# Performance work log

Measured on AMD Instinct MI355X. Metric: run time of the kernel, lower is better.

Reference implementation:

```python
import jax, jax.numpy as jnp
from jax import lax
import numpy as np

C = 64
K = 3  # kernel_size
PAD = K // 2


def setup_inputs() -> dict:
    key = jax.random.key(0)
    k1, k2, k3, k4, k5 = jax.random.split(key, 5)
    B, N, H, W = 2, 16, 96, 96
    x = jax.random.normal(k1, (B, C, N, H, W), dtype=jnp.float32)
    # offset conv: Conv2d(C, 2K, kernel=(1,K)) -> 1D conv weight (2K, C, K)
    w_off = jax.random.normal(k2, (2 * K, C, K), dtype=jnp.float32) * 0.05
    b_off = jax.random.normal(k3, (2 * K,), dtype=jnp.float32) * 0.05
    # deform conv: DeformConv2d(C, C, kernel=(1,K)) -> weight (C, C, K)
    w_def = jax.random.normal(k4, (C, C, K), dtype=jnp.float32) * (1.0 / np.sqrt(C * K))
    b_def = jax.random.normal(k5, (C,), dtype=jnp.float32) * 0.01
    return {"x": x, "w_off": w_off, "b_off": b_off, "w_def": w_def, "b_def": b_def}


def _deform_fuse(x, w_off, b_off, w_def, b_def):
    B, Cc, N, H, W = x.shape
    M = B * H * W
    # (B,C,N,H,W) -> (B,H,W,C,N) -> (M, C, N); the 'width' axis is the focus axis N
    xm = jnp.transpose(x, (0, 3, 4, 1, 2)).reshape(M, Cc, N)

    # offset-predicting 1D conv over N, padding K//2 (same)
    offsets = lax.conv_general_dilated(
        xm, w_off, window_strides=(1,), padding=[(PAD, PAD)],
        dimension_numbers=("NCH", "OIH", "NCH"),
    ) + b_off[None, :, None]  # (M, 2K, N)
    # torchvision ordering: per kernel tap j, channel 2j = dy, 2j+1 = dx
    off_y = offsets[:, 0::2]  # (M, K, N)
    off_x = offsets[:, 1::2]  # (M, K, N)

    # base sampling positions along the (width=N) axis: n - pad + j
    pos = (jnp.arange(N, dtype=x.dtype)[None, :] - PAD
           + jnp.arange(K, dtype=x.dtype)[:, None])  # (K, N)
    px = pos[None] + off_x                            # (M, K, N)
    x0 = jnp.floor(px)
    fx = px - x0                                      # fractional part
    x0i = x0.astype(jnp.int32)
    x1i = x0i + 1
    v0 = ((x0i >= 0) & (x0i < N)).astype(x.dtype)
    v1 = ((x1i >= 0) & (x1i < N)).astype(x.dtype)
    c0 = jnp.clip(x0i, 0, N - 1)
    c1 = jnp.clip(x1i, 0, N - 1)

    # gather along N per row: (C,N) indexed by (K,N) -> (C,K,N)
    gather = jax.vmap(lambda xr, idx: xr[:, idx])
    g0 = gather(xm, c0) * (v0 * (1.0 - fx))[:, None]   # (M, C, K, N)
    g1 = gather(xm, c1) * (v1 * fx)[:, None]
    # height dim is size 1: bilinear weight along y collapses to relu(1-|dy|)
    wy = jnp.maximum(jnp.array(0.0, x.dtype), 1.0 - jnp.abs(off_y))[:, None]  # (M,1,K,N)
    val = (g0 + g1) * wy                               # (M, C, K, N)

    out = jnp.einsum("ock,mckn->mon", w_def, val) + b_def[None, :, None]  # (M, C, N)
    out = out.reshape(B, H, W, Cc, N)
    return jnp.transpose(out, (0, 3, 4, 1, 2))         # (B, C, N, H, W)


def reference(x, w_off, b_off, w_def, b_def):
    return _deform_fuse(x, w_off, b_off, w_def, b_def)
```

## Files before the change

### kernel.cpp

```cpp
#include <hip/hip_runtime.h>
#include <stdint.h>


typedef __attribute__((ext_vector_type(8))) short short8;
typedef __attribute__((ext_vector_type(4))) float f32x4;
typedef __attribute__((ext_vector_type(2))) float f32x2;
typedef __attribute__((ext_vector_type(4))) unsigned int u32x4;

#define XT_OFF   0
#define XG_OFF   36864
#define OFFS_OFF 36864
#define LDS_BYTES 69632

__device__ __forceinline__ short f2bf(float f) {
  union { float f; uint32_t u; } v; v.f = f;
  uint32_t r = (v.u + 0x7FFFu + ((v.u >> 16) & 1u)) >> 16;
  return (short)r;
}
__device__ __forceinline__ float asf(uint32_t u) {
  union { uint32_t u; float f; } v; v.u = u; return v.f;
}
__device__ __forceinline__ uint32_t cvt_pk_bf16(float lo, float hi) {
  uint32_t d;
  asm("v_cvt_pk_bf16_f32 %0, %1, %2" : "=v"(d) : "v"(lo), "v"(hi));
  return d;
}

__global__ __launch_bounds__(256) void prep_kernel(
    const float* __restrict__ w_off, const float* __restrict__ w_def, short8* __restrict__ ws)
{
  int gid = blockIdx.x * 256 + threadIdx.x;
  if (gid < 1536) {
    int mt = gid / 384, ks = (gid % 384) >> 6, ll = gid & 63;
    int m = mt * 16 + (ll & 15), rgq = ll >> 4;
    short8 v;
    #pragma unroll
    for (int jj = 0; jj < 8; ++jj) {
      int kk = ks * 32 + rgq * 8 + jj;
      int c = kk & 63, k3 = kk >> 6;
      v[jj] = f2bf(w_def[m * 192 + c * 3 + k3]);
    }
    ws[gid] = v;
  } else if (gid < 1920) {
    int q = gid - 1536;
    int ks = q >> 6, ll = q & 63;
    int m = ll & 15, rgq = ll >> 4;
    short8 v;
    #pragma unroll
    for (int jj = 0; jj < 8; ++jj) {
      int kk = ks * 32 + rgq * 8 + jj;
      int c = kk & 63, k3 = kk >> 6;
      v[jj] = (m < 6) ? f2bf(w_off[m * 192 + c * 3 + k3]) : (short)0;
    }
    ws[gid] = v;
  }
}

__global__ __launch_bounds__(512, 4) void deform_main(
    const float* __restrict__ x, const float* __restrict__ b_off,
    const float* __restrict__ b_def, const short8* __restrict__ wfr,
    float* __restrict__ out)
{
  extern __shared__ char smem[];
  uint16_t* xst = (uint16_t*)(smem + XG_OFF);
  float* offs   = (float*)(smem + OFFS_OFF);

  const int t = threadIdx.x, wv = t >> 6, l = t & 63, col = l & 15, rg = l >> 4;
  const int tn = blockIdx.x;
  const int wt = tn % 6, bh = tn / 6;
  const int h = bh % 96, b = bh / 96, w0 = wt * 16;
  const float* xb = x + (size_t)b * 9437184 + h * 96 + w0;

  #pragma unroll
  for (int i = 0; i < 8; ++i) {
    int r = (t >> 2) + i * 128, quad = t & 3;
    float4 v = *(const float4*)(xb + (size_t)r * 9216 + quad * 4);
    uint2 pk;
    pk.x = cvt_pk_bf16(v.x, v.y);
    pk.y = cvt_pk_bf16(v.z, v.w);
    *(uint2*)(xst + r * 16 + quad * 4) = pk;
  }
  __syncthreads();

  #pragma unroll
  for (int i = 0; i < 4; ++i) {
    int item = t + 512 * i;
    int pos = item & 255, cg = item >> 8;
    short8 vv;
    #pragma unroll
    for (int jj = 0; jj < 8; ++jj) vv[jj] = (short)xst[(cg * 8 + jj) * 256 + pos];
    *(short8*)(smem + XT_OFF + pos * 144 + cg * 16) = vv;
  }
  __syncthreads();

  {
    f32x4 cacc[2] = {{0.f,0.f,0.f,0.f},{0.f,0.f,0.f,0.f}};
    const short8 zero = {0,0,0,0,0,0,0,0};
    #pragma unroll
    for (int ks = 0; ks < 6; ++ks) {
      short8 av = wfr[1536 + ks * 64 + l];
      int k3 = ks >> 1;
      #pragma unroll
      for (int nt2 = 0; nt2 < 2; ++nt2) {
        int n = wv * 2 + nt2;
        int row = n + k3 - 1;
        bool valid = (row >= 0) && (row < 16);
        int rcl = min(max(row, 0), 15);
        short8 bv = *(short8*)(smem + XT_OFF + (rcl * 16 + col) * 144 + rg * 16 + (ks & 1) * 64);
        bv = valid ? bv : zero;
        cacc[nt2] = __builtin_amdgcn_mfma_f32_16x16x32_bf16(av, bv, cacc[nt2], 0, 0, 0);
      }
    }
    #pragma unroll
    for (int nt2 = 0; nt2 < 2; ++nt2) {
      int pos = (wv * 2 + nt2) * 16 + col;
      #pragma unroll
      for (int r = 0; r < 4; ++r) {
        int rowo = rg * 4 + r;
        if (rowo < 6) offs[rowo * 256 + pos] = cacc[nt2][r];
      }
    }
  }

  float a0v[3][2], a1v[3][2]; int rb[3][2];
  #pragma unroll
  for (int k = 0; k < 3; ++k) {
    #pragma unroll
    for (int nt2 = 0; nt2 < 2; ++nt2) {
      int n = wv * 2 + nt2;
      int pos = n * 16 + col;
      float oy = offs[(2 * k) * 256 + pos] + b_off[2 * k];
      float ox = offs[(2 * k + 1) * 256 + pos] + b_off[2 * k + 1];
      float px = (float)(n - 1 + k) + ox;
      float x0f = floorf(px);
      float fx = px - x0f;
      int x0 = (int)x0f;
      float wy = fmaxf(0.f, 1.f - fabsf(oy));
      float wt1v = fx * wy;
      float wt0v = wy - wt1v;
      float a0, a1; int r0;
      if (x0 >= 0 && x0 < 15)  { r0 = x0; a0 = wt0v; a1 = wt1v; }
      else if (x0 == 15)       { r0 = 14; a0 = 0.f;  a1 = wt0v; }
      else if (x0 == -1)       { r0 = 0;  a0 = wt1v; a1 = 0.f;  }
      else                     { r0 = 0;  a0 = 0.f;  a1 = 0.f;  }
      a0v[k][nt2] = a0; a1v[k][nt2] = a1;
      rb[k][nt2] = (r0 * 16 + col) * 144;
    }
  }

  f32x4 acc[4][2];
  #pragma unroll
  for (int mt = 0; mt < 4; ++mt) {
    float4 bd = *(const float4*)(b_def + mt * 16 + rg * 4);
    #pragma unroll
    for (int nt2 = 0; nt2 < 2; ++nt2) {
      acc[mt][nt2][0] = bd.x; acc[mt][nt2][1] = bd.y;
      acc[mt][nt2][2] = bd.z; acc[mt][nt2][3] = bd.w;
    }
  }
  #pragma unroll
  for (int k3 = 0; k3 < 3; ++k3) {
    #pragma unroll
    for (int ks2 = 0; ks2 < 2; ++ks2) {
      int ks = k3 * 2 + ks2;
      short8 A[4];
      #pragma unroll
      for (int mt = 0; mt < 4; ++mt) A[mt] = wfr[(mt * 6 + ks) * 64 + l];
      #pragma unroll
      for (int nt2 = 0; nt2 < 2; ++nt2) {
        const char* base = smem + XT_OFF + rb[k3][nt2] + rg * 16 + ks2 * 64;
        u32x4 x0 = *(const u32x4*)base;
        u32x4 x1 = *(const u32x4*)(base + 2304);
        f32x2 A0 = {a0v[k3][nt2], a0v[k3][nt2]};
        f32x2 A1 = {a1v[k3][nt2], a1v[k3][nt2]};
        union { uint32_t w[4]; short8 s; } bu;
        #pragma unroll
        for (int q = 0; q < 4; ++q) {
          uint32_t u0 = x0[q], u1 = x1[q];
          f32x2 X0 = { asf(u0 << 16), asf(u0 & 0xffff0000u) };
          f32x2 X1 = { asf(u1 << 16), asf(u1 & 0xffff0000u) };
          f32x2 R = A0 * X0 + A1 * X1;
          bu.w[q] = cvt_pk_bf16(R.x, R.y);
        }
        short8 bv = bu.s;
        #pragma unroll
        for (int mt = 0; mt < 4; ++mt)
          acc[mt][nt2] = __builtin_amdgcn_mfma_f32_16x16x32_bf16(A[mt], bv, acc[mt][nt2], 0, 0, 0);
      }
    }
  }

  float* ob = out + (size_t)b * 9437184 + h * 96 + w0;
  #pragma unroll
  for (int mt = 0; mt < 4; ++mt) {
    #pragma unroll
    for (int nt2 = 0; nt2 < 2; ++nt2) {
      int n = wv * 2 + nt2;
      float* o0 = ob + (size_t)((mt * 16 + rg * 4) * 16 + n) * 9216 + col;
      #pragma unroll
      for (int r = 0; r < 4; ++r)
        o0[(size_t)r * 147456] = acc[mt][nt2][r];
    }
  }
}

extern "C" void kernel_launch(void* const* d_in, const int* in_sizes, int n_in,
                              void* d_out, int out_size, void* d_ws, size_t ws_size,
                              hipStream_t stream) {
  (void)in_sizes; (void)n_in; (void)ws_size; (void)out_size;
  const float* x     = (const float*)d_in[0];
  const float* w_off = (const float*)d_in[1];
  const float* b_off = (const float*)d_in[2];
  const float* w_def = (const float*)d_in[3];
  const float* b_def = (const float*)d_in[4];
  float* out = (float*)d_out;
  short8* wfr = (short8*)d_ws;

  (void)hipFuncSetAttribute((const void*)deform_main,
                            hipFuncAttributeMaxDynamicSharedMemorySize, LDS_BYTES);
  prep_kernel<<<dim3(8), dim3(256), 0, stream>>>(w_off, w_def, wfr);
  deform_main<<<dim3(1152), dim3(512), LDS_BYTES, stream>>>(x, b_off, b_def, wfr, out);
}
```

Before: 171.1 us.

## Process two width tiles per block and prefetch the second tile's input

Each block now handles two consecutive 16-wide tiles, so the grid is halved. The second tile's global loads are issued into registers while the first tile is being computed, overlapping memory latency with MFMA work. The offsets buffer is moved to its own LDS region so it no longer aliases the staging area, which raises LDS usage and may lower occupancy. Holding the prefetched float4 registers also adds register pressure.

```diff
diff --git a/kernel.cpp b/kernel.cpp
--- a/kernel.cpp
+++ b/kernel.cpp
@@ -9,8 +9,8 @@
 
 #define XT_OFF   0
 #define XG_OFF   36864
-#define OFFS_OFF 36864
-#define LDS_BYTES 69632
+#define OFFS_OFF 69632
+#define LDS_BYTES 75776
 
 __device__ __forceinline__ short f2bf(float f) {
   union { float f; uint32_t u; } v; v.f = f;
@@ -67,140 +67,165 @@
 
   const int t = threadIdx.x, wv = t >> 6, l = t & 63, col = l & 15, rg = l >> 4;
   const int tn = blockIdx.x;
-  const int wt = tn % 6, bh = tn / 6;
-  const int h = bh % 96, b = bh / 96, w0 = wt * 16;
+  const int wt2 = tn % 3, bh = tn / 3;
+  const int h = bh % 96, b = bh / 96, w0 = wt2 * 32;
   const float* xb = x + (size_t)b * 9437184 + h * 96 + w0;
+  float* ob       = out + (size_t)b * 9437184 + h * 96 + w0;
+
+  float4 v[8];
 
   #pragma unroll
   for (int i = 0; i < 8; ++i) {
     int r = (t >> 2) + i * 128, quad = t & 3;
-    float4 v = *(const float4*)(xb + (size_t)r * 9216 + quad * 4);
-    uint2 pk;
-    pk.x = cvt_pk_bf16(v.x, v.y);
-    pk.y = cvt_pk_bf16(v.z, v.w);
-    *(uint2*)(xst + r * 16 + quad * 4) = pk;
+    v[i] = *(const float4*)(xb + (size_t)r * 9216 + quad * 4);
   }
-  __syncthreads();
 
   #pragma unroll
-  for (int i = 0; i < 4; ++i) {
-    int item = t + 512 * i;
-    int pos = item & 255, cg = item >> 8;
-    short8 vv;
-    #pragma unroll
-    for (int jj = 0; jj < 8; ++jj) vv[jj] = (short)xst[(cg * 8 + jj) * 256 + pos];
-    *(short8*)(smem + XT_OFF + pos * 144 + cg * 16) = vv;
-  }
-  __syncthreads();
-
-  {
-    f32x4 cacc[2] = {{0.f,0.f,0.f,0.f},{0.f,0.f,0.f,0.f}};
-    const short8 zero = {0,0,0,0,0,0,0,0};
-    #pragma unroll
-    for (int ks = 0; ks < 6; ++ks) {
-      short8 av = wfr[1536 + ks * 64 + l];
-      int k3 = ks >> 1;
+  for (int j = 0; j < 2; ++j) {
+    #pragma unroll
+    for (int i = 0; i < 8; ++i) {
+      int r = (t >> 2) + i * 128, quad = t & 3;
+      uint2 pk;
+      pk.x = cvt_pk_bf16(v[i].x, v[i].y);
+      pk.y = cvt_pk_bf16(v[i].z, v[i].w);
+      *(uint2*)(xst + r * 16 + quad * 4) = pk;
+    }
+    __syncthreads();
+
+    #pragma unroll
+    for (int i = 0; i < 4; ++i) {
+      int item = t + 512 * i;
+      int pos = item & 255, cg = item >> 8;
+      short8 vv;
+      #pragma unroll
+      for (int jj = 0; jj < 8; ++jj) vv[jj] = (short)xst[(cg * 8 + jj) * 256 + pos];
+      *(short8*)(smem + XT_OFF + pos * 144 + cg * 16) = vv;
+    }
+    __syncthreads();
+
+    if (j == 0) {
+      #pragma unroll
+      for (int i = 0; i < 8; ++i) {
+        int r = (t >> 2) + i * 128, quad = t & 3;
+        v[i] = *(const float4*)(xb + 16 + (size_t)r * 9216 + quad * 4);
+      }
+      __builtin_amdgcn_sched_barrier(0);
+    }
+
+    {
+      f32x4 cacc[2] = {{0.f,0.f,0.f,0.f},{0.f,0.f,0.f,0.f}};
+      const short8 zero = {0,0,0,0,0,0,0,0};
+      #pragma unroll
+      for (int ks = 0; ks < 6; ++ks) {
+        short8 av = wfr[1536 + ks * 64 + l];
+        int k3 = ks >> 1;
+        #pragma unroll
+        for (int nt2 = 0; nt2 < 2; ++nt2) {
+          int n = wv * 2 + nt2;
+          int row = n + k3 - 1;
+          bool valid = (row >= 0) && (row < 16);
+          int rcl = min(max(row, 0), 15);
+          short8 bv = *(short8*)(smem + XT_OFF + (rcl * 16 + col) * 144 + rg * 16 + (ks & 1) * 64);
+          bv = valid ? bv : zero;
+          cacc[nt2] = __builtin_amdgcn_mfma_f32_16x16x32_bf16(av, bv, cacc[nt2], 0, 0, 0);
+        }
+      }
+      #pragma unroll
+      for (int nt2 = 0; nt2 < 2; ++nt2) {
+        int pos = (wv * 2 + nt2) * 16 + col;
+        #pragma unroll
+        for (int r = 0; r < 4; ++r) {
+          int rowo = rg * 4 + r;
+          if (rowo < 6) offs[rowo * 256 + pos] = cacc[nt2][r];
+        }
+      }
+    }
+
+    float a0v[3][2], a1v[3][2]; int rb[3][2];
+    #pragma unroll
+    for (int k = 0; k < 3; ++k) {
       #pragma unroll
       for (int nt2 = 0; nt2 < 2; ++nt2) {
         int n = wv * 2 + nt2;
-        int row = n + k3 - 1;
-        bool valid = (row >= 0) && (row < 16);
-        int rcl = min(max(row, 0), 15);
-        short8 bv = *(short8*)(smem + XT_OFF + (rcl * 16 + col) * 144 + rg * 16 + (ks & 1) * 64);
-        bv = valid ? bv : zero;
-        cacc[nt2] = __builtin_amdgcn_mfma_f32_16x16x32_bf16(av, bv, cacc[nt2], 0, 0, 0);
-      }
-    }
-    #pragma unroll
-    for (int nt2 = 0; nt2 < 2; ++nt2) {
-      int pos = (wv * 2 + nt2) * 16 + col;
-      #pragma unroll
-      for (int r = 0; r < 4; ++r) {
-        int rowo = rg * 4 + r;
-        if (rowo < 6) offs[rowo * 256 + pos] = cacc[nt2][r];
-      }
-    }
-  }
-
-  float a0v[3][2], a1v[3][2]; int rb[3][2];
-  #pragma unroll
-  for (int k = 0; k < 3; ++k) {
-    #pragma unroll
-    for (int nt2 = 0; nt2 < 2; ++nt2) {
-      int n = wv * 2 + nt2;
-      int pos = n * 16 + col;
-      float oy = offs[(2 * k) * 256 + pos] + b_off[2 * k];
-      float ox = offs[(2 * k + 1) * 256 + pos] + b_off[2 * k + 1];
-      float px = (float)(n - 1 + k) + ox;
-      float x0f = floorf(px);
-      float fx = px - x0f;
-      int x0 = (int)x0f;
-      float wy = fmaxf(0.f, 1.f - fabsf(oy));
-      float wt1v = fx * wy;
-      float wt0v = wy - wt1v;
-      float a0, a1; int r0;
-      if (x0 >= 0 && x0 < 15)  { r0 = x0; a0 = wt0v; a1 = wt1v; }
-      else if (x0 == 15)       { r0 = 14; a0 = 0.f;  a1 = wt0v; }
-      else if (x0 == -1)       { r0 = 0;  a0 = wt1v; a1 = 0.f;  }
-      else                     { r0 = 0;  a0 = 0.f;  a1 = 0.f;  }
-      a0v[k][nt2] = a0; a1v[k][nt2] = a1;
-      rb[k][nt2] = (r0 * 16 + col) * 144;
-    }
-  }
-
-  f32x4 acc[4][2];
-  #pragma unroll
-  for (int mt = 0; mt < 4; ++mt) {
-    float4 bd = *(const float4*)(b_def + mt * 16 + rg * 4);
-    #pragma unroll
-    for (int nt2 = 0; nt2 < 2; ++nt2) {
-      acc[mt][nt2][0] = bd.x; acc[mt][nt2][1] = bd.y;
-      acc[mt][nt2][2] = bd.z; acc[mt][nt2][3] = bd.w;
-    }
-  }
-  #pragma unroll
-  for (int k3 = 0; k3 < 3; ++k3) {
-    #pragma unroll
-    for (int ks2 = 0; ks2 < 2; ++ks2) {
-      int ks = k3 * 2 + ks2;
-      short8 A[4];
-      #pragma unroll
-      for (int mt = 0; mt < 4; ++mt) A[mt] = wfr[(mt * 6 + ks) * 64 + l];
+        int pos = n * 16 + col;
+        float oy = offs[(2 * k) * 256 + pos] + b_off[2 * k];
+        float ox = offs[(2 * k + 1) * 256 + pos] + b_off[2 * k + 1];
+        float px = (float)(n - 1 + k) + ox;
+        float x0f = floorf(px);
+        float fx = px - x0f;
+        int x0 = (int)x0f;
+        float wy = fmaxf(0.f, 1.f - fabsf(oy));
+        float wt1v = fx * wy;
+        float wt0v = wy - wt1v;
+        float a0, a1; int r0;
+        if (x0 >= 0 && x0 < 15)  { r0 = x0; a0 = wt0v; a1 = wt1v; }
+        else if (x0 == 15)       { r0 = 14; a0 = 0.f;  a1 = wt0v; }
+        else if (x0 == -1)       { r0 = 0;  a0 = wt1v; a1 = 0.f;  }
+        else                     { r0 = 0;  a0 = 0.f;  a1 = 0.f;  }
+        a0v[k][nt2] = a0; a1v[k][nt2] = a1;
+        rb[k][nt2] = (r0 * 16 + col) * 144;
+      }
+    }
+
+    f32x4 acc[4][2];
+    #pragma unroll
+    for (int mt = 0; mt < 4; ++mt) {
+      float4 bd = *(const float4*)(b_def + mt * 16 + rg * 4);
       #pragma unroll
       for (int nt2 = 0; nt2 < 2; ++nt2) {
-        const char* base = smem + XT_OFF + rb[k3][nt2] + rg * 16 + ks2 * 64;
-        u32x4 x0 = *(const u32x4*)base;
-        u32x4 x1 = *(const u32x4*)(base + 2304);
-        f32x2 A0 = {a0v[k3][nt2], a0v[k3][nt2]};
-        f32x2 A1 = {a1v[k3][nt2], a1v[k3][nt2]};
-        union { uint32_t w[4]; short8 s; } bu;
-        #pragma unroll
-        for (int q = 0; q < 4; ++q) {
-          uint32_t u0 = x0[q], u1 = x1[q];
-          f32x2 X0 = { asf(u0 << 16), asf(u0 & 0xffff0000u) };
-          f32x2 X1 = { asf(u1 << 16), asf(u1 & 0xffff0000u) };
-          f32x2 R = A0 * X0 + A1 * X1;
-          bu.w[q] = cvt_pk_bf16(R.x, R.y);
-        }
-        short8 bv = bu.s;
-        #pragma unroll
-        for (int mt = 0; mt < 4; ++mt)
-          acc[mt][nt2] = __builtin_amdgcn_mfma_f32_16x16x32_bf16(A[mt], bv, acc[mt][nt2], 0, 0, 0);
-      }
-    }
-  }
-
-  float* ob = out + (size_t)b * 9437184 + h * 96 + w0;
-  #pragma unroll
-  for (int mt = 0; mt < 4; ++mt) {
-    #pragma unroll
-    for (int nt2 = 0; nt2 < 2; ++nt2) {
-      int n = wv * 2 + nt2;
-      float* o0 = ob + (size_t)((mt * 16 + rg * 4) * 16 + n) * 9216 + col;
-      #pragma unroll
-      for (int r = 0; r < 4; ++r)
-        o0[(size_t)r * 147456] = acc[mt][nt2][r];
-    }
+        acc[mt][nt2][0] = bd.x; acc[mt][nt2][1] = bd.y;
+        acc[mt][nt2][2] = bd.z; acc[mt][nt2][3] = bd.w;
+      }
+    }
+    #pragma unroll
+    for (int k3 = 0; k3 < 3; ++k3) {
+      #pragma unroll
+      for (int ks2 = 0; ks2 < 2; ++ks2) {
+        int ks = k3 * 2 + ks2;
+        short8 A[4];
+        #pragma unroll
+        for (int mt = 0; mt < 4; ++mt) A[mt] = wfr[(mt * 6 + ks) * 64 + l];
+        #pragma unroll
+        for (int nt2 = 0; nt2 < 2; ++nt2) {
+          const char* base = smem + XT_OFF + rb[k3][nt2] + rg * 16 + ks2 * 64;
+          u32x4 x0 = *(const u32x4*)base;
+          u32x4 x1 = *(const u32x4*)(base + 2304);
+          f32x2 A0 = {a0v[k3][nt2], a0v[k3][nt2]};
+          f32x2 A1 = {a1v[k3][nt2], a1v[k3][nt2]};
+          union { uint32_t w[4]; short8 s; } bu;
+          #pragma unroll
+          for (int q = 0; q < 4; ++q) {
+            uint32_t u0 = x0[q], u1 = x1[q];
+            f32x2 X0 = { asf(u0 << 16), asf(u0 & 0xffff0000u) };
+            f32x2 X1 = { asf(u1 << 16), asf(u1 & 0xffff0000u) };
+            f32x2 R = A0 * X0 + A1 * X1;
+            bu.w[q] = cvt_pk_bf16(R.x, R.y);
+          }
+          short8 bv = bu.s;
+          #pragma unroll
+          for (int mt = 0; mt < 4; ++mt)
+            acc[mt][nt2] = __builtin_amdgcn_mfma_f32_16x16x32_bf16(A[mt], bv, acc[mt][nt2], 0, 0, 0);
+        }
+      }
+    }
+
+    {
+      float* obj = ob + j * 16;
+      #pragma unroll
+      for (int mt = 0; mt < 4; ++mt) {
+        #pragma unroll
+        for (int nt2 = 0; nt2 < 2; ++nt2) {
+          int n = wv * 2 + nt2;
+          float* o0 = obj + (size_t)((mt * 16 + rg * 4) * 16 + n) * 9216 + col;
+          #pragma unroll
+          for (int r = 0; r < 4; ++r)
+            o0[(size_t)r * 147456] = acc[mt][nt2][r];
+        }
+      }
+    }
+
+    if (j == 0)
+      __syncthreads();
   }
 }
 
@@ -219,5 +244,5 @@
   (void)hipFuncSetAttribute((const void*)deform_main,
                             hipFuncAttributeMaxDynamicSharedMemorySize, LDS_BYTES);
   prep_kernel<<<dim3(8), dim3(256), 0, stream>>>(w_off, w_def, wfr);
-  deform_main<<<dim3(1152), dim3(512), LDS_BYTES, stream>>>(x, b_off, b_def, wfr, out);
-}
+  deform_main<<<dim3(576), dim3(512), LDS_BYTES, stream>>>(x, b_off, b_def, wfr, out);
+}
```

Result: slower. 226.7 us (+32.5%).
